# Kernel tuning notes

Hardware: AMD Instinct MI355X
Metric: run time of the kernel (lower is better)

The kernel has to match this reference:

```python
import jax, jax.numpy as jnp
import numpy as np

K = 100000
M = 512

def setup_inputs() -> dict:
    key = jax.random.key(0)
    k1, k2, k3, k4 = jax.random.split(key, 4)
    x = jax.random.normal(k1, (K, M), dtype=jnp.float32)
    # nn.Linear(m, m): weight [m, m], bias [m]
    W = jax.random.normal(k2, (M, M), dtype=jnp.float32) * (1.0 / np.sqrt(M))
    b = jax.random.normal(k3, (M,), dtype=jnp.float32) * 0.01
    # attention vector a: [2m, 1], xavier-normal-like scale
    a = jax.random.normal(k4, (2 * M, 1), dtype=jnp.float32) * np.sqrt(2.0 / (2 * M + 1))
    return {"x": x, "W": W, "b": b, "a": a}

def reference(x, W, b, a):
    # h = Linear(x): [k, m]
    h = x @ W.T + b
    h_mean = jnp.mean(h, axis=0)            # [m]
    a1 = a[:M, 0]                           # [m], applied to h[i]
    a2 = a[M:, 0]                           # [m], applied to h_mean
    # e[i] = a^T cat(h[i], h_mean) -> vectorized as two dot products
    e = h @ a1 + jnp.dot(h_mean, a2)        # [k]
    e = jax.nn.relu(e)
    alpha = jax.nn.softmax(e, axis=0)       # [k]
    # weighted sum of ORIGINAL features (feat = x, pre-linear)
    return jnp.sum(x * alpha[:, None], axis=0)  # [m]
```

## Files before the change

### kernel.cpp

```cpp
#include <hip/hip_runtime.h>
#include <math.h>

#define MM 512
#define KK 100000
#define NB1 1024
#define NW  (NB1 * 4)
#define SSTR 32
#define NOUT 16


__device__ inline float waveSum(float v){
  #pragma unroll
  for(int off = 32; off > 0; off >>= 1) v += __shfl_down(v, off, 64);
  return v;
}
__device__ inline float waveMax(float v){
  #pragma unroll
  for(int off = 32; off > 0; off >>= 1) v = fmaxf(v, __shfl_down(v, off, 64));
  return v;
}
__device__ inline float dot8(float4 x0, float4 x1, float4 v0, float4 v1){
  return x0.x*v0.x + x0.y*v0.y + x0.z*v0.z + x0.w*v0.w
       + x1.x*v1.x + x1.y*v1.y + x1.z*v1.z + x1.w*v1.w;
}

__global__ __launch_bounds__(512) void k_vu(const float* __restrict__ W,
                                            const float* __restrict__ a,
                                            float* __restrict__ v,
                                            float* __restrict__ u){
  int j  = threadIdx.x;
  int k0 = blockIdx.x * 8;
  float pv = 0.f, pu = 0.f;
  #pragma unroll
  for(int kk = 0; kk < 8; kk++){
    float w = W[(size_t)(k0 + kk) * MM + j];
    pv += w * a[k0 + kk];
    pu += w * a[MM + k0 + kk];
  }
  atomicAdd(&v[j], pv);
  atomicAdd(&u[j], pu);
}

__global__ __launch_bounds__(256) void k_pass1(const float* __restrict__ x,
                                               const float* __restrict__ vv,
                                               const float* __restrict__ uu,
                                               float* __restrict__ s,
                                               float* __restrict__ sumU,
                                               float* __restrict__ pmax){
  __shared__ float lsum[4];
  __shared__ float lmax[4];
  int tid  = threadIdx.x;
  int lane = tid & 63;
  int wid  = tid >> 6;
  int gw   = blockIdx.x * 4 + wid;

  const float4* v4 = (const float4*)vv;
  const float4* u4 = (const float4*)uu;
  float4 v0 = v4[lane],      v1 = v4[64 + lane];
  float4 u0 = u4[lane],      u1 = u4[64 + lane];
  float accU = 0.f;
  float wmax = -3.4e38f;

  int myN = (KK - 1 - gw) / NW + 1;
  int k = 0;
  for(; k + 8 <= myN; k += 8){
    float d[8];
    #pragma unroll
    for(int r = 0; r < 8; r++){
      size_t row = (size_t)gw + (size_t)(k + r) * NW;
      const float4* xr = (const float4*)(x + row * MM);
      float4 x0 = xr[lane];
      float4 x1 = xr[64 + lane];
      d[r]  = dot8(x0, x1, v0, v1);
      accU += dot8(x0, x1, u0, u1);
    }
    #pragma unroll
    for(int off = 1; off < 64; off <<= 1){
      #pragma unroll
      for(int r = 0; r < 8; r++) d[r] += __shfl_xor(d[r], off, 64);
    }
    float m01 = fmaxf(fmaxf(d[0], d[1]), fmaxf(d[2], d[3]));
    float m23 = fmaxf(fmaxf(d[4], d[5]), fmaxf(d[6], d[7]));
    wmax = fmaxf(wmax, fmaxf(m01, m23));
    float s0 = (lane & 1) ? d[1] : d[0];
    float s1 = (lane & 1) ? d[3] : d[2];
    float s2 = (lane & 1) ? d[5] : d[4];
    float s3 = (lane & 1) ? d[7] : d[6];
    float t0 = (lane & 2) ? s1 : s0;
    float t1 = (lane & 2) ? s3 : s2;
    float rr = (lane & 4) ? t1 : t0;
    if(lane < 8) s[gw * SSTR + k + lane] = rr;
  }
  for(; k < myN; k++){
    size_t row = (size_t)gw + (size_t)k * NW;
    const float4* xr = (const float4*)(x + row * MM);
    float4 x0 = xr[lane];
    float4 x1 = xr[64 + lane];
    float d = dot8(x0, x1, v0, v1);
    accU += dot8(x0, x1, u0, u1);
    #pragma unroll
    for(int off = 1; off < 64; off <<= 1) d += __shfl_xor(d, off, 64);
    wmax = fmaxf(wmax, d);
    if(lane == 0) s[gw * SSTR + k] = d;
  }

  float ws_ = waveSum(accU);
  if(lane == 0){ lsum[wid] = ws_; lmax[wid] = wmax; }
  __syncthreads();
  if(tid == 0){
    atomicAdd(sumU, lsum[0] + lsum[1] + lsum[2] + lsum[3]);
    pmax[blockIdx.x] = fmaxf(fmaxf(lmax[0], lmax[1]), fmaxf(lmax[2], lmax[3]));
  }
}

__global__ __launch_bounds__(256) void k_pass2(const float* __restrict__ x,
                                               const float* __restrict__ s,
                                               const float* __restrict__ b,
                                               const float* __restrict__ a,
                                               const float* __restrict__ sumU,
                                               const float* __restrict__ pmax,
                                               float* __restrict__ part,
                                               float* __restrict__ Z){
  __shared__ float red[8];
  __shared__ float lw[2048];
  int tid  = threadIdx.x;
  int lane = tid & 63;
  int wid  = tid >> 6;
  int gw   = blockIdx.x * 4 + wid;

  float tp = b[tid]       * (a[tid]       + a[MM + tid])
           + b[tid + 256] * (a[tid + 256] + a[MM + tid + 256]);
  float mx = fmaxf(fmaxf(pmax[tid], pmax[tid + 256]),
                   fmaxf(pmax[tid + 512], pmax[tid + 768]));
  float wsum = waveSum(tp);
  mx = waveMax(mx);
  if(lane == 0){ red[wid] = wsum; red[4 + wid] = mx; }
  __syncthreads();
  float c = sumU[0] * (1.0f / (float)KK) + red[0] + red[1] + red[2] + red[3];
  float m = fmaxf(fmaxf(red[4], red[5]), fmaxf(red[6], red[7]));
  m = fmaxf(0.f, m + c);

  float4 a0 = make_float4(0,0,0,0), a1 = make_float4(0,0,0,0);
  float accZ = 0.f;
  int myN = (KK - 1 - gw) / NW + 1;
  int k = 0;
  for(; k + 8 <= myN; k += 8){
    const float4* s4 = (const float4*)(s + gw * SSTR + k);
    float4 wa = s4[0], wb = s4[1];
    float w[8] = {wa.x, wa.y, wa.z, wa.w, wb.x, wb.y, wb.z, wb.w};
    #pragma unroll
    for(int r = 0; r < 8; r++){
      w[r] = __expf(fmaxf(w[r] + c, 0.f) - m);
      accZ += w[r];
    }
    #pragma unroll
    for(int r = 0; r < 8; r++){
      size_t row = (size_t)gw + (size_t)(k + r) * NW;
      const float4* xr = (const float4*)(x + row * MM);
      float4 x0 = xr[lane];
      float4 x1 = xr[64 + lane];
      a0.x += w[r] * x0.x; a0.y += w[r] * x0.y; a0.z += w[r] * x0.z; a0.w += w[r] * x0.w;
      a1.x += w[r] * x1.x; a1.y += w[r] * x1.y; a1.z += w[r] * x1.z; a1.w += w[r] * x1.w;
    }
  }
  for(; k < myN; k++){
    size_t row = (size_t)gw + (size_t)k * NW;
    float w = __expf(fmaxf(s[gw * SSTR + k] + c, 0.f) - m);
    accZ += w;
    const float4* xr = (const float4*)(x + row * MM);
    float4 x0 = xr[lane];
    float4 x1 = xr[64 + lane];
    a0.x += w * x0.x; a0.y += w * x0.y; a0.z += w * x0.z; a0.w += w * x0.w;
    a1.x += w * x1.x; a1.y += w * x1.y; a1.z += w * x1.z; a1.w += w * x1.w;
  }

  float zw = waveSum(accZ);
  __syncthreads();
  float4* lw4 = (float4*)lw;
  lw4[wid * 128 + lane * 2]     = a0;
  lw4[wid * 128 + lane * 2 + 1] = a1;
  if(lane == 0) red[wid] = zw;
  __syncthreads();
  int l = tid >> 2, q = tid & 3;
  float s0 = lw[0*512 + l*8 + q] + lw[1*512 + l*8 + q]
           + lw[2*512 + l*8 + q] + lw[3*512 + l*8 + q];
  float s1 = lw[0*512 + l*8 + 4 + q] + lw[1*512 + l*8 + 4 + q]
           + lw[2*512 + l*8 + 4 + q] + lw[3*512 + l*8 + 4 + q];
  part[(size_t)blockIdx.x * 512 + tid]       = s0;
  part[(size_t)blockIdx.x * 512 + 256 + tid] = s1;
  if(tid == 0)
    atomicAdd(Z, (red[0] + red[1] + red[2] + red[3]) * (1.0f / 64.0f));
}

__global__ __launch_bounds__(256) void k_out(const float* __restrict__ part,
                                             float* __restrict__ acc,
                                             const float* __restrict__ Z,
                                             int* __restrict__ cnt,
                                             float* __restrict__ out){
  __shared__ int lastf;
  int tid = threadIdx.x;
  const float* p = part + (size_t)blockIdx.x * (NB1 / NOUT) * 512;
  float s0 = 0.f, s1 = 0.f;
  #pragma unroll 8
  for(int bb = 0; bb < NB1 / NOUT; bb++){
    s0 += p[bb * 512 + tid];
    s1 += p[bb * 512 + 256 + tid];
  }
  atomicAdd(&acc[tid],       s0);
  atomicAdd(&acc[tid + 256], s1);
  __threadfence();
  if(tid == 0) lastf = (atomicAdd(cnt, 1) == NOUT - 1) ? 1 : 0;
  __syncthreads();
  if(lastf){
    float z = Z[0];
    float v0 = atomicAdd(&acc[tid],       0.0f);
    float v1 = atomicAdd(&acc[tid + 256], 0.0f);
    out[tid]       = v0 / z;
    out[tid + 256] = v1 / z;
  }
}

extern "C" void kernel_launch(void* const* d_in, const int* in_sizes, int n_in,
                              void* d_out, int out_size, void* d_ws, size_t ws_size,
                              hipStream_t stream) {
  const float* x = (const float*)d_in[0];
  const float* W = (const float*)d_in[1];
  const float* b = (const float*)d_in[2];
  const float* a = (const float*)d_in[3];
  float* ws  = (float*)d_ws;
  float* out = (float*)d_out;

  float* v    = ws;
  float* u    = ws + 512;
  float* sumU = ws + 1024;
  float* Z    = ws + 1025;
  int*   cnt  = (int*)(ws + 1026);
  float* acc  = ws + 1536;
  float* pmax = ws + 2048;
  float* s    = ws + 4096;
  float* part = ws + 196608;

  hipMemsetAsync(ws, 0, 2048 * sizeof(float), stream);

  k_vu   <<<64,   512, 0, stream>>>(W, a, v, u);
  k_pass1<<<NB1,  256, 0, stream>>>(x, v, u, s, sumU, pmax);
  k_pass2<<<NB1,  256, 0, stream>>>(x, s, b, a, sumU, pmax, part, Z);
  k_out  <<<NOUT, 256, 0, stream>>>(part, acc, Z, cnt, out);
}
```

Baseline: 338.0 us.

## Fuse weighted accumulation into first pass with online softmax and ReLU correction

Pass 1 now computes an online-softmax weighted sum of x using unclamped scores, producing per-block partial sums and normalizers. A second kernel rescales those partials to the global max and adds corrections only for rows whose score is clamped by ReLU, rereading just those rows. This aims to cut the second full read of x to roughly the clamped fraction, at the cost of extra exp/FMA work in pass 1, shallower unrolling, and divergent gathers in the correction pass.

```diff
diff --git a/kernel.cpp b/kernel.cpp
--- a/kernel.cpp
+++ b/kernel.cpp
@@ -22,6 +22,12 @@
 __device__ inline float dot8(float4 x0, float4 x1, float4 v0, float4 v1){
   return x0.x*v0.x + x0.y*v0.y + x0.z*v0.z + x0.w*v0.w
        + x1.x*v1.x + x1.y*v1.y + x1.z*v1.z + x1.w*v1.w;
+}
+__device__ inline void fma4(float4& acc, float w, float4 x){
+  acc.x += w * x.x; acc.y += w * x.y; acc.z += w * x.z; acc.w += w * x.w;
+}
+__device__ inline void scale4(float4& v, float s){
+  v.x *= s; v.y *= s; v.z *= s; v.w *= s;
 }
 
 __global__ __launch_bounds__(512) void k_vu(const float* __restrict__ W,
@@ -41,14 +47,18 @@
   atomicAdd(&u[j], pu);
 }
 
-__global__ __launch_bounds__(256) void k_pass1(const float* __restrict__ x,
-                                               const float* __restrict__ vv,
-                                               const float* __restrict__ uu,
-                                               float* __restrict__ s,
-                                               float* __restrict__ sumU,
-                                               float* __restrict__ pmax){
+__global__ __launch_bounds__(256) void k_pass1o(const float* __restrict__ x,
+                                                const float* __restrict__ vv,
+                                                const float* __restrict__ uu,
+                                                float* __restrict__ s,
+                                                float* __restrict__ sumU,
+                                                float* __restrict__ pmax,
+                                                float* __restrict__ part,
+                                                float* __restrict__ zpart){
   __shared__ float lsum[4];
   __shared__ float lmax[4];
+  __shared__ float ezs[4];
+  __shared__ float lw[2048];
   int tid  = threadIdx.x;
   int lane = tid & 63;
   int wid  = tid >> 6;
@@ -59,37 +69,55 @@
   float4 v0 = v4[lane],      v1 = v4[64 + lane];
   float4 u0 = u4[lane],      u1 = u4[64 + lane];
   float accU = 0.f;
-  float wmax = -3.4e38f;
+  float m_w  = -3.4e38f;
+  float Ez   = 0.f;
+  float4 E0 = make_float4(0,0,0,0), E1 = make_float4(0,0,0,0);
 
   int myN = (KK - 1 - gw) / NW + 1;
   int k = 0;
-  for(; k + 8 <= myN; k += 8){
-    float d[8];
-    #pragma unroll
-    for(int r = 0; r < 8; r++){
-      size_t row = (size_t)gw + (size_t)(k + r) * NW;
-      const float4* xr = (const float4*)(x + row * MM);
-      float4 x0 = xr[lane];
-      float4 x1 = xr[64 + lane];
-      d[r]  = dot8(x0, x1, v0, v1);
-      accU += dot8(x0, x1, u0, u1);
-    }
+  for(; k + 4 <= myN; k += 4){
+    size_t r0 = (size_t)gw + (size_t)(k + 0) * NW;
+    size_t r1 = (size_t)gw + (size_t)(k + 1) * NW;
+    size_t r2 = (size_t)gw + (size_t)(k + 2) * NW;
+    size_t r3 = (size_t)gw + (size_t)(k + 3) * NW;
+    const float4* pa = (const float4*)(x + r0 * MM);
+    const float4* pb = (const float4*)(x + r1 * MM);
+    const float4* pc = (const float4*)(x + r2 * MM);
+    const float4* pd = (const float4*)(x + r3 * MM);
+    float4 xa0 = pa[lane], xa1 = pa[64 + lane];
+    float4 xb0 = pb[lane], xb1 = pb[64 + lane];
+    float4 xc0 = pc[lane], xc1 = pc[64 + lane];
+    float4 xd0 = pd[lane], xd1 = pd[64 + lane];
+    float d0 = dot8(xa0, xa1, v0, v1);  accU += dot8(xa0, xa1, u0, u1);
+    float d1 = dot8(xb0, xb1, v0, v1);  accU += dot8(xb0, xb1, u0, u1);
+    float d2 = dot8(xc0, xc1, v0, v1);  accU += dot8(xc0, xc1, u0, u1);
+    float d3 = dot8(xd0, xd1, v0, v1);  accU += dot8(xd0, xd1, u0, u1);
     #pragma unroll
     for(int off = 1; off < 64; off <<= 1){
-      #pragma unroll
-      for(int r = 0; r < 8; r++) d[r] += __shfl_xor(d[r], off, 64);
-    }
-    float m01 = fmaxf(fmaxf(d[0], d[1]), fmaxf(d[2], d[3]));
-    float m23 = fmaxf(fmaxf(d[4], d[5]), fmaxf(d[6], d[7]));
-    wmax = fmaxf(wmax, fmaxf(m01, m23));
-    float s0 = (lane & 1) ? d[1] : d[0];
-    float s1 = (lane & 1) ? d[3] : d[2];
-    float s2 = (lane & 1) ? d[5] : d[4];
-    float s3 = (lane & 1) ? d[7] : d[6];
-    float t0 = (lane & 2) ? s1 : s0;
-    float t1 = (lane & 2) ? s3 : s2;
-    float rr = (lane & 4) ? t1 : t0;
-    if(lane < 8) s[gw * SSTR + k + lane] = rr;
+      d0 += __shfl_xor(d0, off, 64);
+      d1 += __shfl_xor(d1, off, 64);
+      d2 += __shfl_xor(d2, off, 64);
+      d3 += __shfl_xor(d3, off, 64);
+    }
+    float g = fmaxf(fmaxf(d0, d1), fmaxf(d2, d3));
+    if(g > m_w){
+      float sc = __expf(m_w - g);
+      scale4(E0, sc); scale4(E1, sc); Ez *= sc;
+      m_w = g;
+    }
+    float w0 = __expf(d0 - m_w);
+    float w1 = __expf(d1 - m_w);
+    float w2 = __expf(d2 - m_w);
+    float w3 = __expf(d3 - m_w);
+    Ez += w0 + w1 + w2 + w3;
+    fma4(E0, w0, xa0); fma4(E1, w0, xa1);
+    fma4(E0, w1, xb0); fma4(E1, w1, xb1);
+    fma4(E0, w2, xc0); fma4(E1, w2, xc1);
+    fma4(E0, w3, xd0); fma4(E1, w3, xd1);
+    float s0 = (lane & 1) ? d1 : d0;
+    float s1 = (lane & 1) ? d3 : d2;
+    float rr = (lane & 2) ? s1 : s0;
+    if(lane < 4) s[gw * SSTR + k + lane] = rr;
   }
   for(; k < myN; k++){
     size_t row = (size_t)gw + (size_t)k * NW;
@@ -100,28 +128,53 @@
     accU += dot8(x0, x1, u0, u1);
     #pragma unroll
     for(int off = 1; off < 64; off <<= 1) d += __shfl_xor(d, off, 64);
-    wmax = fmaxf(wmax, d);
+    if(d > m_w){
+      float sc = __expf(m_w - d);
+      scale4(E0, sc); scale4(E1, sc); Ez *= sc;
+      m_w = d;
+    }
+    float w = __expf(d - m_w);
+    Ez += w;
+    fma4(E0, w, x0); fma4(E1, w, x1);
     if(lane == 0) s[gw * SSTR + k] = d;
   }
 
-  float ws_ = waveSum(accU);
-  if(lane == 0){ lsum[wid] = ws_; lmax[wid] = wmax; }
-  __syncthreads();
+  float us = waveSum(accU);
+  if(lane == 0){ lsum[wid] = us; lmax[wid] = m_w; }
+  __syncthreads();
+  float m_blk = fmaxf(fmaxf(lmax[0], lmax[1]), fmaxf(lmax[2], lmax[3]));
+  float sc2 = __expf(m_w - m_blk);
+  scale4(E0, sc2); scale4(E1, sc2);
+  if(lane == 0) ezs[wid] = Ez * sc2;
+  float4* lw4 = (float4*)lw;
+  lw4[wid * 128 + lane * 2]     = E0;
+  lw4[wid * 128 + lane * 2 + 1] = E1;
+  __syncthreads();
+  int l = tid >> 2, q = tid & 3;
+  float o0 = lw[0*512 + l*8 + q] + lw[1*512 + l*8 + q]
+           + lw[2*512 + l*8 + q] + lw[3*512 + l*8 + q];
+  float o1 = lw[0*512 + l*8 + 4 + q] + lw[1*512 + l*8 + 4 + q]
+           + lw[2*512 + l*8 + 4 + q] + lw[3*512 + l*8 + 4 + q];
+  part[(size_t)blockIdx.x * 512 + tid]       = o0;
+  part[(size_t)blockIdx.x * 512 + 256 + tid] = o1;
   if(tid == 0){
     atomicAdd(sumU, lsum[0] + lsum[1] + lsum[2] + lsum[3]);
-    pmax[blockIdx.x] = fmaxf(fmaxf(lmax[0], lmax[1]), fmaxf(lmax[2], lmax[3]));
-  }
-}
-
-__global__ __launch_bounds__(256) void k_pass2(const float* __restrict__ x,
-                                               const float* __restrict__ s,
-                                               const float* __restrict__ b,
-                                               const float* __restrict__ a,
-                                               const float* __restrict__ sumU,
-                                               const float* __restrict__ pmax,
-                                               float* __restrict__ part,
-                                               float* __restrict__ Z){
+    pmax[blockIdx.x]  = m_blk;
+    zpart[blockIdx.x] = ezs[0] + ezs[1] + ezs[2] + ezs[3];
+  }
+}
+
+__global__ __launch_bounds__(256) void k_corr(const float* __restrict__ x,
+                                              const float* __restrict__ s,
+                                              const float* __restrict__ b,
+                                              const float* __restrict__ a,
+                                              const float* __restrict__ sumU,
+                                              const float* __restrict__ pmax,
+                                              float* __restrict__ part,
+                                              const float* __restrict__ zpart,
+                                              float* __restrict__ Z){
   __shared__ float red[8];
+  __shared__ float czs[4];
   __shared__ float lw[2048];
   int tid  = threadIdx.x;
   int lane = tid & 63;
@@ -136,60 +189,83 @@
   mx = waveMax(mx);
   if(lane == 0){ red[wid] = wsum; red[4 + wid] = mx; }
   __syncthreads();
-  float c = sumU[0] * (1.0f / (float)KK) + red[0] + red[1] + red[2] + red[3];
-  float m = fmaxf(fmaxf(red[4], red[5]), fmaxf(red[6], red[7]));
-  m = fmaxf(0.f, m + c);
-
-  float4 a0 = make_float4(0,0,0,0), a1 = make_float4(0,0,0,0);
-  float accZ = 0.f;
+  float c  = sumU[0] * (1.0f / (float)KK) + red[0] + red[1] + red[2] + red[3];
+  float mg = fmaxf(fmaxf(red[4], red[5]), fmaxf(red[6], red[7]));
+  float M  = fmaxf(0.f, mg + c);
+  float eM = __expf(-M);
+
+  float4 C0 = make_float4(0,0,0,0), C1 = make_float4(0,0,0,0);
+  float Cz = 0.f;
   int myN = (KK - 1 - gw) / NW + 1;
-  int k = 0;
-  for(; k + 8 <= myN; k += 8){
-    const float4* s4 = (const float4*)(s + gw * SSTR + k);
-    float4 wa = s4[0], wb = s4[1];
-    float w[8] = {wa.x, wa.y, wa.z, wa.w, wb.x, wb.y, wb.z, wb.w};
-    #pragma unroll
-    for(int r = 0; r < 8; r++){
-      w[r] = __expf(fmaxf(w[r] + c, 0.f) - m);
-      accZ += w[r];
-    }
-    #pragma unroll
-    for(int r = 0; r < 8; r++){
-      size_t row = (size_t)gw + (size_t)(k + r) * NW;
-      const float4* xr = (const float4*)(x + row * MM);
-      float4 x0 = xr[lane];
-      float4 x1 = xr[64 + lane];
-      a0.x += w[r] * x0.x; a0.y += w[r] * x0.y; a0.z += w[r] * x0.z; a0.w += w[r] * x0.w;
-      a1.x += w[r] * x1.x; a1.y += w[r] * x1.y; a1.z += w[r] * x1.z; a1.w += w[r] * x1.w;
-    }
-  }
-  for(; k < myN; k++){
-    size_t row = (size_t)gw + (size_t)k * NW;
-    float w = __expf(fmaxf(s[gw * SSTR + k] + c, 0.f) - m);
-    accZ += w;
-    const float4* xr = (const float4*)(x + row * MM);
-    float4 x0 = xr[lane];
-    float4 x1 = xr[64 + lane];
-    a0.x += w * x0.x; a0.y += w * x0.y; a0.z += w * x0.z; a0.w += w * x0.w;
-    a1.x += w * x1.x; a1.y += w * x1.y; a1.z += w * x1.z; a1.w += w * x1.w;
-  }
-
-  float zw = waveSum(accZ);
+  const float4* s4 = (const float4*)(s + gw * SSTR);
+  #pragma unroll
+  for(int g2 = 0; g2 < 7; g2++){
+    int kb = g2 * 4;
+    if(kb >= myN) break;
+    float4 sv = s4[g2];
+    {
+      int k = kb + 0;
+      float t = sv.x + c;
+      if(k < myN && t < 0.f){
+        float kap = eM - __expf(t - M);
+        size_t row = (size_t)gw + (size_t)k * NW;
+        const float4* xr = (const float4*)(x + row * MM);
+        float4 x0 = xr[lane], x1 = xr[64 + lane];
+        fma4(C0, kap, x0); fma4(C1, kap, x1); Cz += kap;
+      }
+    }
+    {
+      int k = kb + 1;
+      float t = sv.y + c;
+      if(k < myN && t < 0.f){
+        float kap = eM - __expf(t - M);
+        size_t row = (size_t)gw + (size_t)k * NW;
+        const float4* xr = (const float4*)(x + row * MM);
+        float4 x0 = xr[lane], x1 = xr[64 + lane];
+        fma4(C0, kap, x0); fma4(C1, kap, x1); Cz += kap;
+      }
+    }
+    {
+      int k = kb + 2;
+      float t = sv.z + c;
+      if(k < myN && t < 0.f){
+        float kap = eM - __expf(t - M);
+        size_t row = (size_t)gw + (size_t)k * NW;
+        const float4* xr = (const float4*)(x + row * MM);
+        float4 x0 = xr[lane], x1 = xr[64 + lane];
+        fma4(C0, kap, x0); fma4(C1, kap, x1); Cz += kap;
+      }
+    }
+    {
+      int k = kb + 3;
+      float t = sv.w + c;
+      if(k < myN && t < 0.f){
+        float kap = eM - __expf(t - M);
+        size_t row = (size_t)gw + (size_t)k * NW;
+        const float4* xr = (const float4*)(x + row * MM);
+        float4 x0 = xr[lane], x1 = xr[64 + lane];
+        fma4(C0, kap, x0); fma4(C1, kap, x1); Cz += kap;
+      }
+    }
+  }
+
   __syncthreads();
   float4* lw4 = (float4*)lw;
-  lw4[wid * 128 + lane * 2]     = a0;
-  lw4[wid * 128 + lane * 2 + 1] = a1;
-  if(lane == 0) red[wid] = zw;
+  lw4[wid * 128 + lane * 2]     = C0;
+  lw4[wid * 128 + lane * 2 + 1] = C1;
+  if(lane == 0) czs[wid] = Cz;
   __syncthreads();
   int l = tid >> 2, q = tid & 3;
-  float s0 = lw[0*512 + l*8 + q] + lw[1*512 + l*8 + q]
+  float o0 = lw[0*512 + l*8 + q] + lw[1*512 + l*8 + q]
            + lw[2*512 + l*8 + q] + lw[3*512 + l*8 + q];
-  float s1 = lw[0*512 + l*8 + 4 + q] + lw[1*512 + l*8 + 4 + q]
+  float o1 = lw[0*512 + l*8 + 4 + q] + lw[1*512 + l*8 + 4 + q]
            + lw[2*512 + l*8 + 4 + q] + lw[3*512 + l*8 + 4 + q];
-  part[(size_t)blockIdx.x * 512 + tid]       = s0;
-  part[(size_t)blockIdx.x * 512 + 256 + tid] = s1;
+  float scB = __expf(c - M + pmax[blockIdx.x]);
+  size_t base = (size_t)blockIdx.x * 512;
+  part[base + tid]       = part[base + tid]       * scB + o0;
+  part[base + 256 + tid] = part[base + 256 + tid] * scB + o1;
   if(tid == 0)
-    atomicAdd(Z, (red[0] + red[1] + red[2] + red[3]) * (1.0f / 64.0f));
+    atomicAdd(Z, czs[0] + czs[1] + czs[2] + czs[3] + scB * zpart[blockIdx.x]);
 }
 
 __global__ __launch_bounds__(256) void k_out(const float* __restrict__ part,
@@ -230,20 +306,21 @@
   float* ws  = (float*)d_ws;
   float* out = (float*)d_out;
 
-  float* v    = ws;
-  float* u    = ws + 512;
-  float* sumU = ws + 1024;
-  float* Z    = ws + 1025;
-  int*   cnt  = (int*)(ws + 1026);
-  float* acc  = ws + 1536;
-  float* pmax = ws + 2048;
-  float* s    = ws + 4096;
-  float* part = ws + 196608;
+  float* v     = ws;
+  float* u     = ws + 512;
+  float* sumU  = ws + 1024;
+  float* Z     = ws + 1025;
+  int*   cnt   = (int*)(ws + 1026);
+  float* acc   = ws + 1536;
+  float* pmax  = ws + 2048;
+  float* zpart = ws + 3072;
+  float* s     = ws + 4096;
+  float* part  = ws + 196608;
 
   hipMemsetAsync(ws, 0, 2048 * sizeof(float), stream);
 
-  k_vu   <<<64,   512, 0, stream>>>(W, a, v, u);
-  k_pass1<<<NB1,  256, 0, stream>>>(x, v, u, s, sumU, pmax);
-  k_pass2<<<NB1,  256, 0, stream>>>(x, s, b, a, sumU, pmax, part, Z);
-  k_out  <<<NOUT, 256, 0, stream>>>(part, acc, Z, cnt, out);
-}
+  k_vu    <<<64,   512, 0, stream>>>(W, a, v, u);
+  k_pass1o<<<NB1,  256, 0, stream>>>(x, v, u, s, sumU, pmax, part, zpart);
+  k_corr  <<<NB1,  256, 0, stream>>>(x, s, b, a, sumU, pmax, part, zpart, Z);
+  k_out   <<<NOUT, 256, 0, stream>>>(part, acc, Z, cnt, out);
+}
```

Result: faster. 326.7 us (-3.4%).
